# Performance work log

Hardware: AMD Instinct MI355X
Metric: run time of the kernel (lower is better)

Reference implementation:

```python
import jax, jax.numpy as jnp
import numpy as np

N, E, SEQ, IN, HID, OUT = 2048, 65536, 5, 32, 64, 16
EPS = 1e-5


def setup_inputs() -> dict:
    ks = jax.random.split(jax.random.key(0), 16)
    def w(k, shape):
        return jax.random.normal(k, shape, jnp.float32) / np.float32(np.sqrt(shape[0]))
    z = lambda n: jnp.zeros((n,), jnp.float32)
    return dict(
        x=jax.random.normal(ks[0], (SEQ, N, IN), jnp.float32),
        edge_weight=jax.random.uniform(ks[1], (E,), jnp.float32),
        Wcz=w(ks[2], (IN, HID)), bcz=z(HID), Wlz=w(ks[3], (2 * HID, HID)), blz=z(HID),
        Wcr=w(ks[4], (IN, HID)), bcr=z(HID), Wlr=w(ks[5], (2 * HID, HID)), blr=z(HID),
        Wch=w(ks[6], (IN, HID)), bch=z(HID), Wlh=w(ks[7], (2 * HID, HID)), blh=z(HID),
        Wred=w(ks[8], (SEQ * HID, HID)), bred=z(HID),
        Wc1=w(ks[9], (HID, HID)), bc1=z(HID), Wc2=w(ks[10], (HID, HID)), bc2=z(HID),
        g1=jnp.ones((HID,), jnp.float32), be1=z(HID),
        g2=jnp.ones((HID,), jnp.float32), be2=z(HID),
        Wout=w(ks[11], (HID, OUT)), bout=z(OUT),
        Wi1=w(ks[12], (2 * HID, HID)), bi1=z(HID),
        Wi2=w(ks[13], (HID, 1)), bi2=z(1),
        edge_index=jax.random.randint(ks[14], (2, E), 0, N),
    )


def _layer_norm(h, g, b):
    mu = jnp.mean(h, -1, keepdims=True)
    var = jnp.mean((h - mu) ** 2, -1, keepdims=True)
    return (h - mu) * jax.lax.rsqrt(var + EPS) * g + b


def _forward(x, edge_weight, Wcz, bcz, Wlz, blz, Wcr, bcr, Wlr, blr,
             Wch, bch, Wlh, blh, Wred, bred, Wc1, bc1, Wc2, bc2,
             g1, be1, g2, be2, Wout, bout, Wi1, bi1, Wi2, bi2, edge_index):
    src, dst = edge_index[0], edge_index[1]
    # GCN symmetric normalization with self-loops (weight 1.0); shared by all convs.
    deg = jax.ops.segment_sum(edge_weight, dst, num_segments=N) + 1.0
    dinv = jax.lax.rsqrt(deg)
    norm = dinv[src] * edge_weight * dinv[dst]  # [E]
    dself = dinv * dinv                          # [N] self-loop coefficient

    def gcn(h, W, b):
        hw = h @ W
        agg = jax.ops.segment_sum(norm[:, None] * hw[src], dst, num_segments=N)
        return agg + dself[:, None] * hw + b

    # TGCN per timestep. The original passes no hidden state, so H resets to 0
    # each call: H_t = (1 - Z) * tanh(candidate); reset gate R is multiplied by
    # H=0 and has no effect (its params get zero gradient, matching torch).
    hs = []
    for t in range(SEQ):  # SEQ=5, fixed small loop
        Zg = jax.nn.sigmoid(gcn(x[t], Wcz, bcz) @ Wlz[:HID] + blz)
        Ht = jnp.tanh(gcn(x[t], Wch, bch) @ Wlh[:HID] + blh)
        hs.append((1.0 - Zg) * Ht)
    h = jnp.stack(hs, axis=1).reshape(N, SEQ * HID)
    h = h @ Wred + bred
    emb = h  # intermediate embeddings for the interaction predictor
    h = gcn(h, Wc1, bc1)
    h = jax.nn.relu(_layer_norm(h, g1, be1))  # dropout = identity in eval
    h = gcn(h, Wc2, bc2)
    h = jax.nn.relu(_layer_norm(h, g2, be2))
    node_pred = h @ Wout + bout
    # InteractionPredictor: cat([e_i, e_j]) @ Wi1 == e_i @ Wi1[:H] + e_j @ Wi1[H:]
    a = emb @ Wi1[:HID]
    bj = emb @ Wi1[HID:]
    hp = jax.nn.relu(a[:, None, :] + bj[None, :, :] + bi1)  # [N, N, HID]
    scores = (hp @ Wi2)[..., 0] + bi2[0]                     # [N, N]
    return node_pred, scores


def reference(x, edge_index, edge_weight, Wcz, bcz, Wlz, blz, Wcr, bcr, Wlr, blr,
              Wch, bch, Wlh, blh, Wred, bred, Wc1, bc1, Wc2, bc2,
              g1, be1, g2, be2, Wout, bout, Wi1, bi1, Wi2, bi2):
    return _forward(x, edge_weight, Wcz, bcz, Wlz, blz, Wcr, bcr, Wlr, blr,
                    Wch, bch, Wlh, blh, Wred, bred, Wc1, bc1, Wc2, bc2,
                    g1, be1, g2, be2, Wout, bout, Wi1, bi1, Wi2, bi2, edge_index)
```

## Files before the change

kernel.cpp:

```cpp
#include <hip/hip_runtime.h>
#include <math.h>

#define N_NODES 2048
#define N_EDGES 65536
#define SEQL 5
#define IN_F 32
#define HID 64
#define OUT_F 16
#define LN_EPS 1e-5f

__global__ void k_deg(const int* __restrict__ ei, const float* __restrict__ ew,
                      float* __restrict__ deg, int* __restrict__ cnt){
    int e = blockIdx.x * 256 + threadIdx.x;
    if (e < N_EDGES){
        int d = ei[N_EDGES + e];
        atomicAdd(&deg[d], ew[e]);
        atomicAdd(&cnt[d], 1);
    }
}

__global__ void k_scan_wcomb(const float* __restrict__ deg, const int* __restrict__ cnt,
                             float* __restrict__ dinv, float* __restrict__ dself, int* __restrict__ rowptr,
                             const float* __restrict__ Wcz, const float* __restrict__ Wlz,
                             const float* __restrict__ bcz, const float* __restrict__ blz,
                             const float* __restrict__ Wch, const float* __restrict__ Wlh,
                             const float* __restrict__ bch, const float* __restrict__ blh,
                             float* __restrict__ Wzp, float* __restrict__ Whp, float* __restrict__ bUV){
    int b = blockIdx.x, t = threadIdx.x;
    if (b == 0){
        __shared__ int s[1024];
        int n0 = 2*t, n1 = 2*t + 1;
        float d0 = deg[n0] + 1.f, d1 = deg[n1] + 1.f;
        float i0 = 1.f / sqrtf(d0), i1 = 1.f / sqrtf(d1);
        dinv[n0] = i0; dinv[n1] = i1;
        dself[n0] = i0*i0; dself[n1] = i1*i1;
        int a0 = cnt[n0], a1 = cnt[n1];
        s[t] = a0 + a1;
        __syncthreads();
        for (int off = 1; off < 1024; off <<= 1){
            int v = (t >= off) ? s[t - off] : 0;
            __syncthreads();
            s[t] += v;
            __syncthreads();
        }
        int pe = (t == 0) ? 0 : s[t-1];
        rowptr[n0] = pe;
        rowptr[n1] = pe + a0;
        if (t == 1023) rowptr[2048] = s[1023];
    } else {
        const float* Wc = (b == 1) ? Wcz : Wch;
        const float* Wl = (b == 1) ? Wlz : Wlh;
        const float* bc = (b == 1) ? bcz : bch;
        const float* bl = (b == 1) ? blz : blh;
        float* Wp = (b == 1) ? Wzp : Whp;
        for (int idx = t; idx < IN_F*HID; idx += 1024){
            int i = idx >> 6, f = idx & 63;
            float s = 0.f;
            for (int k = 0; k < HID; ++k) s += Wc[i*HID+k] * Wl[k*HID+f];
            Wp[idx] = s;
        }
        if (t < HID){
            float s = bl[t];
            for (int k = 0; k < HID; ++k) s += bc[k] * Wl[k*HID+t];
            bUV[(b-1)*HID + t] = s;
        }
    }
}

__global__ void k_csr(const int* __restrict__ ei, const float* __restrict__ ew,
                      const float* __restrict__ dinv, const int* __restrict__ rowptr,
                      int* __restrict__ fill, int* __restrict__ csrc, float* __restrict__ cnrm){
    int e = blockIdx.x * 256 + threadIdx.x;
    if (e < N_EDGES){
        int s = ei[e], d = ei[N_EDGES + e];
        int pos = rowptr[d] + atomicAdd(&fill[d], 1);
        csrc[pos] = s;
        cnrm[pos] = dinv[s] * ew[e] * dinv[d];
    }
}

__global__ __launch_bounds__(256) void k_aggx(const float* __restrict__ x, const float* __restrict__ dself,
        const int* __restrict__ rowptr, const int* __restrict__ csrc, const float* __restrict__ cnrm,
        float* __restrict__ aggX){
    int n = blockIdx.x;
    int tid = threadIdx.x;
    int slot = tid >> 5, f = tid & 31;
    __shared__ float part[8][SEQL][IN_F];
    float acc[SEQL] = {0.f, 0.f, 0.f, 0.f, 0.f};
    int beg = rowptr[n], end = rowptr[n+1];
    for (int p = beg + slot; p < end; p += 8){
        int s = csrc[p]; float c = cnrm[p];
        #pragma unroll
        for (int t = 0; t < SEQL; ++t)
            acc[t] += c * x[(t*N_NODES + s)*IN_F + f];
    }
    #pragma unroll
    for (int t = 0; t < SEQL; ++t) part[slot][t][f] = acc[t];
    __syncthreads();
    if (tid < SEQL*IN_F){
        int t = tid >> 5, ff = tid & 31;
        float s = dself[n] * x[(t*N_NODES + n)*IN_F + ff];
        #pragma unroll
        for (int sl = 0; sl < 8; ++sl) s += part[sl][t][ff];
        aggX[n*(SEQL*IN_F) + tid] = s;
    }
}

__global__ __launch_bounds__(320) void k_gate2(const float* __restrict__ aggX, const float* __restrict__ bUV,
        const float* __restrict__ Wzp, const float* __restrict__ Whp,
        const float* __restrict__ Wred, const float* __restrict__ bred,
        const float* __restrict__ Wi1, const float* __restrict__ bi1, const float* __restrict__ Wc1,
        float* __restrict__ emb, float* __restrict__ ag, float* __restrict__ bjp,
        float* __restrict__ hw1){
    int n = blockIdx.x;
    int f = threadIdx.x & 63;
    int t = threadIdx.x >> 6;
    __shared__ float axs[SEQL][IN_F];
    __shared__ float hs[SEQL][HID];
    __shared__ float part[SEQL][HID];
    if (threadIdx.x < SEQL*IN_F) ((float*)axs)[threadIdx.x] = aggX[n*(SEQL*IN_F) + threadIdx.x];
    __syncthreads();
    float zz = bUV[f], hh = bUV[HID + f];
    #pragma unroll
    for (int i = 0; i < IN_F; ++i){
        float a = axs[t][i];
        zz += a * Wzp[i*HID + f];
        hh += a * Whp[i*HID + f];
    }
    float z = 1.f / (1.f + expf(-zz));
    hs[t][f] = (1.f - z) * tanhf(hh);
    __syncthreads();
    float pp = 0.f;
    #pragma unroll
    for (int k = 0; k < HID; ++k) pp += hs[t][k] * Wred[(t*HID + k)*HID + f];
    part[t][f] = pp;
    __syncthreads();
    if (t == 0){
        float hred = bred[f] + part[0][f] + part[1][f] + part[2][f] + part[3][f] + part[4][f];
        emb[n*HID + f] = hred;
        hs[0][f] = hred;
    }
    __syncthreads();
    if (t < 3){
        const float* W = (t == 0) ? Wi1 : (t == 1) ? (Wi1 + HID*HID) : Wc1;
        float acc = (t == 1) ? bi1[f] : 0.f;
        #pragma unroll
        for (int k = 0; k < HID; ++k) acc += hs[0][k] * W[k*HID + f];
        float* O = (t == 0) ? ag : (t == 1) ? bjp : hw1;
        O[n*HID + f] = acc;
    }
}

__global__ __launch_bounds__(256) void k_gcn1(
                       const float* __restrict__ hw1, const float* __restrict__ dself,
                       const int* __restrict__ rowptr, const int* __restrict__ csrc, const float* __restrict__ cnrm,
                       const float* __restrict__ bc1, const float* __restrict__ g1, const float* __restrict__ be1,
                       const float* __restrict__ Wc2, float* __restrict__ hw2){
    int n = blockIdx.x;
    int f = threadIdx.x & 63;
    int w = threadIdx.x >> 6;
    int beg = rowptr[n], end = rowptr[n+1];
    __shared__ float red[4][HID];
    __shared__ float hsh[HID];
    float agg = 0.f;
    for (int p = beg + w; p < end; p += 4) agg += cnrm[p] * hw1[csrc[p]*HID + f];
    red[w][f] = agg;
    __syncthreads();
    if (w == 0){
        float g = red[0][f] + red[1][f] + red[2][f] + red[3][f]
                + dself[n] * hw1[n*HID + f] + bc1[f];
        float sum = g;
        for (int o = 32; o > 0; o >>= 1) sum += __shfl_xor(sum, o, 64);
        float mu = sum * (1.f/64.f);
        float d = g - mu;
        float vs = d * d;
        for (int o = 32; o > 0; o >>= 1) vs += __shfl_xor(vs, o, 64);
        float var = vs * (1.f/64.f);
        float h = d * (1.f / sqrtf(var + LN_EPS)) * g1[f] + be1[f];
        hsh[f] = fmaxf(h, 0.f);
    }
    __syncthreads();
    float s = 0.f;
    #pragma unroll
    for (int k = 0; k < 16; ++k) s += hsh[w*16 + k] * Wc2[(w*16 + k)*HID + f];
    red[w][f] = s;
    __syncthreads();
    if (w == 0) hw2[n*HID + f] = red[0][f] + red[1][f] + red[2][f] + red[3][f];
}

__global__ __launch_bounds__(256) void k_gcn2(
                       const float* __restrict__ hw2, const float* __restrict__ dself,
                       const int* __restrict__ rowptr, const int* __restrict__ csrc, const float* __restrict__ cnrm,
                       const float* __restrict__ bc2, const float* __restrict__ g2, const float* __restrict__ be2,
                       const float* __restrict__ Wout, const float* __restrict__ bout, float* __restrict__ outp){
    int n = blockIdx.x;
    int f = threadIdx.x & 63;
    int w = threadIdx.x >> 6;
    int beg = rowptr[n], end = rowptr[n+1];
    __shared__ float red[4][HID];
    __shared__ float hsh[HID];
    float agg = 0.f;
    for (int p = beg + w; p < end; p += 4) agg += cnrm[p] * hw2[csrc[p]*HID + f];
    red[w][f] = agg;
    __syncthreads();
    if (w == 0){
        float g = red[0][f] + red[1][f] + red[2][f] + red[3][f]
                + dself[n] * hw2[n*HID + f] + bc2[f];
        float sum = g;
        for (int o = 32; o > 0; o >>= 1) sum += __shfl_xor(sum, o, 64);
        float mu = sum * (1.f/64.f);
        float d = g - mu;
        float vs = d * d;
        for (int o = 32; o > 0; o >>= 1) vs += __shfl_xor(vs, o, 64);
        float var = vs * (1.f/64.f);
        float h = d * (1.f / sqrtf(var + LN_EPS)) * g2[f] + be2[f];
        hsh[f] = fmaxf(h, 0.f);
    }
    __syncthreads();
    if (w == 0 && f < OUT_F){
        float s = bout[f];
        #pragma unroll
        for (int k = 0; k < HID; ++k) s += hsh[k] * Wout[k*OUT_F + f];
        outp[n*OUT_F + f] = s;
    }
}

__global__ __launch_bounds__(256) void k_scores(const float* __restrict__ ag, const float* __restrict__ bjp,
                         const float* __restrict__ Wi2, const float* __restrict__ bi2,
                         float* __restrict__ outs){
    __shared__ __align__(16) float bs[64][68];
    __shared__ __align__(16) float as[16][68];
    __shared__ __align__(16) float wv[64];
    int tid = threadIdx.x;
    int j0 = blockIdx.x * 64;
    int i0 = blockIdx.y * 16;
    for (int idx = tid; idx < 1024; idx += 256){
        int jj = idx >> 4, c = idx & 15;
        float4 v = *(const float4*)&bjp[(j0 + jj)*HID + c*4];
        *(float4*)&bs[jj][c*4] = v;
    }
    {   int ii = tid >> 4, c = tid & 15;
        float4 v = *(const float4*)&ag[(i0 + ii)*HID + c*4];
        *(float4*)&as[ii][c*4] = v;
    }
    if (tid < 64) wv[tid] = Wi2[tid];
    __syncthreads();
    int tj = tid & 63;
    int w = tid >> 6;
    float bi2v = bi2[0];
    float acc0 = 0.f, acc1 = 0.f, acc2 = 0.f, acc3 = 0.f;
    #pragma unroll
    for (int c = 0; c < 16; ++c){
        float4 bv = *(float4*)&bs[tj][c*4];
        float4 w4 = *(float4*)&wv[c*4];
        float4 a0 = *(float4*)&as[w*4 + 0][c*4];
        float4 a1 = *(float4*)&as[w*4 + 1][c*4];
        float4 a2 = *(float4*)&as[w*4 + 2][c*4];
        float4 a3 = *(float4*)&as[w*4 + 3][c*4];
        acc0 += fmaxf(a0.x+bv.x,0.f)*w4.x + fmaxf(a0.y+bv.y,0.f)*w4.y
              + fmaxf(a0.z+bv.z,0.f)*w4.z + fmaxf(a0.w+bv.w,0.f)*w4.w;
        acc1 += fmaxf(a1.x+bv.x,0.f)*w4.x + fmaxf(a1.y+bv.y,0.f)*w4.y
              + fmaxf(a1.z+bv.z,0.f)*w4.z + fmaxf(a1.w+bv.w,0.f)*w4.w;
        acc2 += fmaxf(a2.x+bv.x,0.f)*w4.x + fmaxf(a2.y+bv.y,0.f)*w4.y
              + fmaxf(a2.z+bv.z,0.f)*w4.z + fmaxf(a2.w+bv.w,0.f)*w4.w;
        acc3 += fmaxf(a3.x+bv.x,0.f)*w4.x + fmaxf(a3.y+bv.y,0.f)*w4.y
              + fmaxf(a3.z+bv.z,0.f)*w4.z + fmaxf(a3.w+bv.w,0.f)*w4.w;
    }
    long ro = (long)(i0 + w*4) * N_NODES + j0 + tj;
    outs[ro                ] = acc0 + bi2v;
    outs[ro +     N_NODES  ] = acc1 + bi2v;
    outs[ro + 2L* N_NODES  ] = acc2 + bi2v;
    outs[ro + 3L* N_NODES  ] = acc3 + bi2v;
}

extern "C" void kernel_launch(void* const* d_in, const int* in_sizes, int n_in,
                              void* d_out, int out_size, void* d_ws, size_t ws_size,
                              hipStream_t stream){
    const float* x   = (const float*)d_in[0];
    const float* ew  = (const float*)d_in[1];
    const float* Wcz = (const float*)d_in[2];  const float* bcz = (const float*)d_in[3];
    const float* Wlz = (const float*)d_in[4];  const float* blz = (const float*)d_in[5];
    const float* Wch = (const float*)d_in[10]; const float* bch = (const float*)d_in[11];
    const float* Wlh = (const float*)d_in[12]; const float* blh = (const float*)d_in[13];
    const float* Wred= (const float*)d_in[14]; const float* bred= (const float*)d_in[15];
    const float* Wc1 = (const float*)d_in[16]; const float* bc1 = (const float*)d_in[17];
    const float* Wc2 = (const float*)d_in[18]; const float* bc2 = (const float*)d_in[19];
    const float* g1  = (const float*)d_in[20]; const float* be1 = (const float*)d_in[21];
    const float* g2  = (const float*)d_in[22]; const float* be2 = (const float*)d_in[23];
    const float* Wout= (const float*)d_in[24]; const float* bout= (const float*)d_in[25];
    const float* Wi1 = (const float*)d_in[26]; const float* bi1 = (const float*)d_in[27];
    const float* Wi2 = (const float*)d_in[28]; const float* bi2 = (const float*)d_in[29];
    const int*  ei  = (const int*)d_in[30];

    char* w = (char*)d_ws;
    float* deg    = (float*)(w + 0);
    int*   cnt    = (int*)  (w + 8192);
    int*   fill   = (int*)  (w + 16384);
    int*   rowptr = (int*)  (w + 24576);
    float* dinv   = (float*)(w + 36864);
    float* dself  = (float*)(w + 45056);
    int*   csrc   = (int*)  (w + 53248);
    float* cnrm   = (float*)(w + 315392);
    float* Wzp    = (float*)(w + 577536);
    float* Whp    = (float*)(w + 585728);
    float* bUV    = (float*)(w + 593920);
    float* aggX   = (float*)(w + 595968);
    float* emb    = (float*)(w + 1906688);
    float* ag     = emb + N_NODES*HID;
    float* bjp    = ag  + N_NODES*HID;
    float* hw1    = bjp + N_NODES*HID;
    float* hw2    = hw1 + N_NODES*HID;

    hipMemsetAsync(d_ws, 0, 24576, stream);
    k_deg<<<N_EDGES/256, 256, 0, stream>>>(ei, ew, deg, cnt);
    k_scan_wcomb<<<3, 1024, 0, stream>>>(deg, cnt, dinv, dself, rowptr,
                                         Wcz, Wlz, bcz, blz, Wch, Wlh, bch, blh,
                                         Wzp, Whp, bUV);
    k_csr<<<N_EDGES/256, 256, 0, stream>>>(ei, ew, dinv, rowptr, fill, csrc, cnrm);
    k_aggx<<<N_NODES, 256, 0, stream>>>(x, dself, rowptr, csrc, cnrm, aggX);
    k_gate2<<<N_NODES, 320, 0, stream>>>(aggX, bUV, Wzp, Whp, Wred, bred, Wi1, bi1, Wc1,
                                         emb, ag, bjp, hw1);
    k_gcn1<<<N_NODES, 256, 0, stream>>>(hw1, dself, rowptr, csrc, cnrm, bc1, g1, be1, Wc2, hw2);
    k_gcn2<<<N_NODES, 256, 0, stream>>>(hw2, dself, rowptr, csrc, cnrm, bc2, g2, be2, Wout, bout,
                                        (float*)d_out);
    dim3 sg(N_NODES/64, N_NODES/16);
    k_scores<<<sg, 256, 0, stream>>>(ag, bjp, Wi2, bi2, (float*)d_out + N_NODES*OUT_F);
}
```

Before: 218.8 us.

## Fuse all stages into one persistent cooperative kernel with grid syncs

Replaces the memset and eight separate kernel launches with a single cooperative kernel of 256 blocks of 512 threads. Stages are separated by grid.sync(), and each block loops over 8 nodes or tiles per stage. The aggX and emb intermediates are no longer written to global memory; the gate computation reads aggregated features from shared memory. This removes launch gaps and the memset, but adds grid-wide barriers and gives low occupancy (256 blocks) for the gather and score phases, which could cost throughput.

```diff
diff --git a/kernel.cpp b/kernel.cpp
--- a/kernel.cpp
+++ b/kernel.cpp
@@ -1,5 +1,8 @@
 #include <hip/hip_runtime.h>
+#include <hip/hip_cooperative_groups.h>
 #include <math.h>
+
+namespace cg = cooperative_groups;
 
 #define N_NODES 2048
 #define N_EDGES 65536
@@ -8,321 +11,332 @@
 #define HID 64
 #define OUT_F 16
 #define LN_EPS 1e-5f
-
-__global__ void k_deg(const int* __restrict__ ei, const float* __restrict__ ew,
-                      float* __restrict__ deg, int* __restrict__ cnt){
-    int e = blockIdx.x * 256 + threadIdx.x;
-    if (e < N_EDGES){
-        int d = ei[N_EDGES + e];
-        atomicAdd(&deg[d], ew[e]);
-        atomicAdd(&cnt[d], 1);
-    }
-}
-
-__global__ void k_scan_wcomb(const float* __restrict__ deg, const int* __restrict__ cnt,
-                             float* __restrict__ dinv, float* __restrict__ dself, int* __restrict__ rowptr,
-                             const float* __restrict__ Wcz, const float* __restrict__ Wlz,
-                             const float* __restrict__ bcz, const float* __restrict__ blz,
-                             const float* __restrict__ Wch, const float* __restrict__ Wlh,
-                             const float* __restrict__ bch, const float* __restrict__ blh,
-                             float* __restrict__ Wzp, float* __restrict__ Whp, float* __restrict__ bUV){
-    int b = blockIdx.x, t = threadIdx.x;
-    if (b == 0){
-        __shared__ int s[1024];
-        int n0 = 2*t, n1 = 2*t + 1;
-        float d0 = deg[n0] + 1.f, d1 = deg[n1] + 1.f;
-        float i0 = 1.f / sqrtf(d0), i1 = 1.f / sqrtf(d1);
-        dinv[n0] = i0; dinv[n1] = i1;
-        dself[n0] = i0*i0; dself[n1] = i1*i1;
-        int a0 = cnt[n0], a1 = cnt[n1];
-        s[t] = a0 + a1;
+#define NBLK 256
+#define NTHR 512
+
+struct Params {
+    const float *x, *ew;
+    const float *Wcz, *bcz, *Wlz, *blz;
+    const float *Wch, *bch, *Wlh, *blh;
+    const float *Wred, *bred, *Wc1, *bc1, *Wc2, *bc2;
+    const float *g1, *be1, *g2, *be2, *Wout, *bout;
+    const float *Wi1, *bi1, *Wi2, *bi2;
+    const int *ei;
+    float *deg; int *cnt; int *fill; int *rowptr;
+    float *dinv, *dself; int *csrc; float *cnrm;
+    float *Wzp, *Whp, *bUV;
+    float *ag, *bjp, *hw1, *hw2;
+    float *outp, *outs;
+};
+
+__global__ __launch_bounds__(NTHR) void k_mega(Params P){
+    cg::grid_group grid = cg::this_grid();
+    const int tid = threadIdx.x, blk = blockIdx.x;
+    const int gid = blk * NTHR + tid;
+    __shared__ float LP[6656];
+
+    if (gid < N_NODES){ P.deg[gid] = 0.f; P.cnt[gid] = 0; P.fill[gid] = 0; }
+    grid.sync();
+
+    if (gid < N_EDGES){
+        int d = P.ei[N_EDGES + gid];
+        atomicAdd(&P.deg[d], P.ew[gid]);
+        atomicAdd(&P.cnt[d], 1);
+    }
+    grid.sync();
+
+    if (blk == 0){
+        int* sc = (int*)LP;
+        int base = tid * 4;
+        int c0 = P.cnt[base], c1 = P.cnt[base+1], c2 = P.cnt[base+2], c3 = P.cnt[base+3];
+        int ts = c0 + c1 + c2 + c3;
+        sc[tid] = ts;
         __syncthreads();
-        for (int off = 1; off < 1024; off <<= 1){
-            int v = (t >= off) ? s[t - off] : 0;
-            __syncthreads();
-            s[t] += v;
-            __syncthreads();
-        }
-        int pe = (t == 0) ? 0 : s[t-1];
-        rowptr[n0] = pe;
-        rowptr[n1] = pe + a0;
-        if (t == 1023) rowptr[2048] = s[1023];
-    } else {
-        const float* Wc = (b == 1) ? Wcz : Wch;
-        const float* Wl = (b == 1) ? Wlz : Wlh;
-        const float* bc = (b == 1) ? bcz : bch;
-        const float* bl = (b == 1) ? blz : blh;
-        float* Wp = (b == 1) ? Wzp : Whp;
-        for (int idx = t; idx < IN_F*HID; idx += 1024){
+        for (int off = 1; off < NTHR; off <<= 1){
+            int v = (tid >= off) ? sc[tid - off] : 0;
+            __syncthreads();
+            sc[tid] += v;
+            __syncthreads();
+        }
+        int exc = sc[tid] - ts;
+        P.rowptr[base]   = exc;
+        P.rowptr[base+1] = exc + c0;
+        P.rowptr[base+2] = exc + c0 + c1;
+        P.rowptr[base+3] = exc + c0 + c1 + c2;
+        if (tid == NTHR-1) P.rowptr[N_NODES] = sc[tid];
+    } else if (blk == 1 || blk == 2){
+        const float* Wc = (blk == 1) ? P.Wcz : P.Wch;
+        const float* Wl = (blk == 1) ? P.Wlz : P.Wlh;
+        const float* bc = (blk == 1) ? P.bcz : P.bch;
+        const float* bl = (blk == 1) ? P.blz : P.blh;
+        float* Wp = (blk == 1) ? P.Wzp : P.Whp;
+        for (int idx = tid; idx < IN_F*HID; idx += NTHR){
             int i = idx >> 6, f = idx & 63;
             float s = 0.f;
             for (int k = 0; k < HID; ++k) s += Wc[i*HID+k] * Wl[k*HID+f];
             Wp[idx] = s;
         }
-        if (t < HID){
-            float s = bl[t];
-            for (int k = 0; k < HID; ++k) s += bc[k] * Wl[k*HID+t];
-            bUV[(b-1)*HID + t] = s;
-        }
-    }
-}
-
-__global__ void k_csr(const int* __restrict__ ei, const float* __restrict__ ew,
-                      const float* __restrict__ dinv, const int* __restrict__ rowptr,
-                      int* __restrict__ fill, int* __restrict__ csrc, float* __restrict__ cnrm){
-    int e = blockIdx.x * 256 + threadIdx.x;
-    if (e < N_EDGES){
-        int s = ei[e], d = ei[N_EDGES + e];
-        int pos = rowptr[d] + atomicAdd(&fill[d], 1);
-        csrc[pos] = s;
-        cnrm[pos] = dinv[s] * ew[e] * dinv[d];
-    }
-}
-
-__global__ __launch_bounds__(256) void k_aggx(const float* __restrict__ x, const float* __restrict__ dself,
-        const int* __restrict__ rowptr, const int* __restrict__ csrc, const float* __restrict__ cnrm,
-        float* __restrict__ aggX){
-    int n = blockIdx.x;
-    int tid = threadIdx.x;
-    int slot = tid >> 5, f = tid & 31;
-    __shared__ float part[8][SEQL][IN_F];
-    float acc[SEQL] = {0.f, 0.f, 0.f, 0.f, 0.f};
-    int beg = rowptr[n], end = rowptr[n+1];
-    for (int p = beg + slot; p < end; p += 8){
-        int s = csrc[p]; float c = cnrm[p];
+        if (tid < HID){
+            float s = bl[tid];
+            for (int k = 0; k < HID; ++k) s += bc[k] * Wl[k*HID+tid];
+            P.bUV[(blk-1)*HID + tid] = s;
+        }
+    } else if (blk == 3){
+        int base = tid * 4;
         #pragma unroll
-        for (int t = 0; t < SEQL; ++t)
-            acc[t] += c * x[(t*N_NODES + s)*IN_F + f];
-    }
-    #pragma unroll
-    for (int t = 0; t < SEQL; ++t) part[slot][t][f] = acc[t];
-    __syncthreads();
-    if (tid < SEQL*IN_F){
-        int t = tid >> 5, ff = tid & 31;
-        float s = dself[n] * x[(t*N_NODES + n)*IN_F + ff];
-        #pragma unroll
-        for (int sl = 0; sl < 8; ++sl) s += part[sl][t][ff];
-        aggX[n*(SEQL*IN_F) + tid] = s;
-    }
-}
-
-__global__ __launch_bounds__(320) void k_gate2(const float* __restrict__ aggX, const float* __restrict__ bUV,
-        const float* __restrict__ Wzp, const float* __restrict__ Whp,
-        const float* __restrict__ Wred, const float* __restrict__ bred,
-        const float* __restrict__ Wi1, const float* __restrict__ bi1, const float* __restrict__ Wc1,
-        float* __restrict__ emb, float* __restrict__ ag, float* __restrict__ bjp,
-        float* __restrict__ hw1){
-    int n = blockIdx.x;
-    int f = threadIdx.x & 63;
-    int t = threadIdx.x >> 6;
-    __shared__ float axs[SEQL][IN_F];
-    __shared__ float hs[SEQL][HID];
-    __shared__ float part[SEQL][HID];
-    if (threadIdx.x < SEQL*IN_F) ((float*)axs)[threadIdx.x] = aggX[n*(SEQL*IN_F) + threadIdx.x];
-    __syncthreads();
-    float zz = bUV[f], hh = bUV[HID + f];
-    #pragma unroll
-    for (int i = 0; i < IN_F; ++i){
-        float a = axs[t][i];
-        zz += a * Wzp[i*HID + f];
-        hh += a * Whp[i*HID + f];
-    }
-    float z = 1.f / (1.f + expf(-zz));
-    hs[t][f] = (1.f - z) * tanhf(hh);
-    __syncthreads();
-    float pp = 0.f;
-    #pragma unroll
-    for (int k = 0; k < HID; ++k) pp += hs[t][k] * Wred[(t*HID + k)*HID + f];
-    part[t][f] = pp;
-    __syncthreads();
-    if (t == 0){
-        float hred = bred[f] + part[0][f] + part[1][f] + part[2][f] + part[3][f] + part[4][f];
-        emb[n*HID + f] = hred;
-        hs[0][f] = hred;
-    }
-    __syncthreads();
-    if (t < 3){
-        const float* W = (t == 0) ? Wi1 : (t == 1) ? (Wi1 + HID*HID) : Wc1;
-        float acc = (t == 1) ? bi1[f] : 0.f;
-        #pragma unroll
-        for (int k = 0; k < HID; ++k) acc += hs[0][k] * W[k*HID + f];
-        float* O = (t == 0) ? ag : (t == 1) ? bjp : hw1;
-        O[n*HID + f] = acc;
-    }
-}
-
-__global__ __launch_bounds__(256) void k_gcn1(
-                       const float* __restrict__ hw1, const float* __restrict__ dself,
-                       const int* __restrict__ rowptr, const int* __restrict__ csrc, const float* __restrict__ cnrm,
-                       const float* __restrict__ bc1, const float* __restrict__ g1, const float* __restrict__ be1,
-                       const float* __restrict__ Wc2, float* __restrict__ hw2){
-    int n = blockIdx.x;
-    int f = threadIdx.x & 63;
-    int w = threadIdx.x >> 6;
-    int beg = rowptr[n], end = rowptr[n+1];
-    __shared__ float red[4][HID];
-    __shared__ float hsh[HID];
-    float agg = 0.f;
-    for (int p = beg + w; p < end; p += 4) agg += cnrm[p] * hw1[csrc[p]*HID + f];
-    red[w][f] = agg;
-    __syncthreads();
-    if (w == 0){
-        float g = red[0][f] + red[1][f] + red[2][f] + red[3][f]
-                + dself[n] * hw1[n*HID + f] + bc1[f];
-        float sum = g;
-        for (int o = 32; o > 0; o >>= 1) sum += __shfl_xor(sum, o, 64);
-        float mu = sum * (1.f/64.f);
-        float d = g - mu;
-        float vs = d * d;
-        for (int o = 32; o > 0; o >>= 1) vs += __shfl_xor(vs, o, 64);
-        float var = vs * (1.f/64.f);
-        float h = d * (1.f / sqrtf(var + LN_EPS)) * g1[f] + be1[f];
-        hsh[f] = fmaxf(h, 0.f);
-    }
-    __syncthreads();
-    float s = 0.f;
-    #pragma unroll
-    for (int k = 0; k < 16; ++k) s += hsh[w*16 + k] * Wc2[(w*16 + k)*HID + f];
-    red[w][f] = s;
-    __syncthreads();
-    if (w == 0) hw2[n*HID + f] = red[0][f] + red[1][f] + red[2][f] + red[3][f];
-}
-
-__global__ __launch_bounds__(256) void k_gcn2(
-                       const float* __restrict__ hw2, const float* __restrict__ dself,
-                       const int* __restrict__ rowptr, const int* __restrict__ csrc, const float* __restrict__ cnrm,
-                       const float* __restrict__ bc2, const float* __restrict__ g2, const float* __restrict__ be2,
-                       const float* __restrict__ Wout, const float* __restrict__ bout, float* __restrict__ outp){
-    int n = blockIdx.x;
-    int f = threadIdx.x & 63;
-    int w = threadIdx.x >> 6;
-    int beg = rowptr[n], end = rowptr[n+1];
-    __shared__ float red[4][HID];
-    __shared__ float hsh[HID];
-    float agg = 0.f;
-    for (int p = beg + w; p < end; p += 4) agg += cnrm[p] * hw2[csrc[p]*HID + f];
-    red[w][f] = agg;
-    __syncthreads();
-    if (w == 0){
-        float g = red[0][f] + red[1][f] + red[2][f] + red[3][f]
-                + dself[n] * hw2[n*HID + f] + bc2[f];
-        float sum = g;
-        for (int o = 32; o > 0; o >>= 1) sum += __shfl_xor(sum, o, 64);
-        float mu = sum * (1.f/64.f);
-        float d = g - mu;
-        float vs = d * d;
-        for (int o = 32; o > 0; o >>= 1) vs += __shfl_xor(vs, o, 64);
-        float var = vs * (1.f/64.f);
-        float h = d * (1.f / sqrtf(var + LN_EPS)) * g2[f] + be2[f];
-        hsh[f] = fmaxf(h, 0.f);
-    }
-    __syncthreads();
-    if (w == 0 && f < OUT_F){
-        float s = bout[f];
-        #pragma unroll
-        for (int k = 0; k < HID; ++k) s += hsh[k] * Wout[k*OUT_F + f];
-        outp[n*OUT_F + f] = s;
-    }
-}
-
-__global__ __launch_bounds__(256) void k_scores(const float* __restrict__ ag, const float* __restrict__ bjp,
-                         const float* __restrict__ Wi2, const float* __restrict__ bi2,
-                         float* __restrict__ outs){
-    __shared__ __align__(16) float bs[64][68];
-    __shared__ __align__(16) float as[16][68];
-    __shared__ __align__(16) float wv[64];
-    int tid = threadIdx.x;
-    int j0 = blockIdx.x * 64;
-    int i0 = blockIdx.y * 16;
-    for (int idx = tid; idx < 1024; idx += 256){
-        int jj = idx >> 4, c = idx & 15;
-        float4 v = *(const float4*)&bjp[(j0 + jj)*HID + c*4];
-        *(float4*)&bs[jj][c*4] = v;
-    }
-    {   int ii = tid >> 4, c = tid & 15;
-        float4 v = *(const float4*)&ag[(i0 + ii)*HID + c*4];
-        *(float4*)&as[ii][c*4] = v;
-    }
-    if (tid < 64) wv[tid] = Wi2[tid];
-    __syncthreads();
-    int tj = tid & 63;
-    int w = tid >> 6;
-    float bi2v = bi2[0];
-    float acc0 = 0.f, acc1 = 0.f, acc2 = 0.f, acc3 = 0.f;
-    #pragma unroll
-    for (int c = 0; c < 16; ++c){
-        float4 bv = *(float4*)&bs[tj][c*4];
-        float4 w4 = *(float4*)&wv[c*4];
-        float4 a0 = *(float4*)&as[w*4 + 0][c*4];
-        float4 a1 = *(float4*)&as[w*4 + 1][c*4];
-        float4 a2 = *(float4*)&as[w*4 + 2][c*4];
-        float4 a3 = *(float4*)&as[w*4 + 3][c*4];
-        acc0 += fmaxf(a0.x+bv.x,0.f)*w4.x + fmaxf(a0.y+bv.y,0.f)*w4.y
-              + fmaxf(a0.z+bv.z,0.f)*w4.z + fmaxf(a0.w+bv.w,0.f)*w4.w;
-        acc1 += fmaxf(a1.x+bv.x,0.f)*w4.x + fmaxf(a1.y+bv.y,0.f)*w4.y
-              + fmaxf(a1.z+bv.z,0.f)*w4.z + fmaxf(a1.w+bv.w,0.f)*w4.w;
-        acc2 += fmaxf(a2.x+bv.x,0.f)*w4.x + fmaxf(a2.y+bv.y,0.f)*w4.y
-              + fmaxf(a2.z+bv.z,0.f)*w4.z + fmaxf(a2.w+bv.w,0.f)*w4.w;
-        acc3 += fmaxf(a3.x+bv.x,0.f)*w4.x + fmaxf(a3.y+bv.y,0.f)*w4.y
-              + fmaxf(a3.z+bv.z,0.f)*w4.z + fmaxf(a3.w+bv.w,0.f)*w4.w;
-    }
-    long ro = (long)(i0 + w*4) * N_NODES + j0 + tj;
-    outs[ro                ] = acc0 + bi2v;
-    outs[ro +     N_NODES  ] = acc1 + bi2v;
-    outs[ro + 2L* N_NODES  ] = acc2 + bi2v;
-    outs[ro + 3L* N_NODES  ] = acc3 + bi2v;
+        for (int k = 0; k < 4; ++k){
+            int i = base + k;
+            float di = 1.f / sqrtf(P.deg[i] + 1.f);
+            P.dinv[i] = di; P.dself[i] = di * di;
+        }
+    }
+    grid.sync();
+
+    if (gid < N_EDGES){
+        int s = P.ei[gid], d = P.ei[N_EDGES + gid];
+        int pos = P.rowptr[d] + atomicAdd(&P.fill[d], 1);
+        P.csrc[pos] = s;
+        P.cnrm[pos] = P.dinv[s] * P.ew[gid] * P.dinv[d];
+    }
+    grid.sync();
+
+    {
+        float* part = LP;
+        float* axs  = LP + 2560;
+        float* hs   = LP + 2720;
+        float* pw   = LP + 3040;
+        float* hemb = LP + 3360;
+        const int slot = tid >> 5, f5 = tid & 31;
+        const int f = tid & 63, t = tid >> 6;
+        for (int rep = 0; rep < 8; ++rep){
+            int n = (rep << 8) + blk;
+            __syncthreads();
+            int beg = P.rowptr[n], end = P.rowptr[n+1];
+            float a0=0.f, a1=0.f, a2=0.f, a3=0.f, a4=0.f;
+            for (int p = beg + slot; p < end; p += 16){
+                int s = P.csrc[p]; float c = P.cnrm[p];
+                a0 += c * P.x[(0*N_NODES + s)*IN_F + f5];
+                a1 += c * P.x[(1*N_NODES + s)*IN_F + f5];
+                a2 += c * P.x[(2*N_NODES + s)*IN_F + f5];
+                a3 += c * P.x[(3*N_NODES + s)*IN_F + f5];
+                a4 += c * P.x[(4*N_NODES + s)*IN_F + f5];
+            }
+            part[(slot*SEQL + 0)*IN_F + f5] = a0;
+            part[(slot*SEQL + 1)*IN_F + f5] = a1;
+            part[(slot*SEQL + 2)*IN_F + f5] = a2;
+            part[(slot*SEQL + 3)*IN_F + f5] = a3;
+            part[(slot*SEQL + 4)*IN_F + f5] = a4;
+            __syncthreads();
+            if (tid < SEQL*IN_F){
+                int tt = tid >> 5, ff = tid & 31;
+                float s = P.dself[n] * P.x[(tt*N_NODES + n)*IN_F + ff];
+                #pragma unroll
+                for (int sl = 0; sl < 16; ++sl) s += part[(sl*SEQL + tt)*IN_F + ff];
+                axs[tt*IN_F + ff] = s;
+            }
+            __syncthreads();
+            if (t < SEQL){
+                float zz = P.bUV[f], hh = P.bUV[HID + f];
+                #pragma unroll
+                for (int i = 0; i < IN_F; ++i){
+                    float a = axs[t*IN_F + i];
+                    zz += a * P.Wzp[i*HID + f];
+                    hh += a * P.Whp[i*HID + f];
+                }
+                float z = 1.f / (1.f + expf(-zz));
+                hs[t*HID + f] = (1.f - z) * tanhf(hh);
+            }
+            __syncthreads();
+            if (t < SEQL){
+                float pp = 0.f;
+                #pragma unroll
+                for (int k = 0; k < HID; ++k) pp += hs[t*HID + k] * P.Wred[(t*HID + k)*HID + f];
+                pw[t*HID + f] = pp;
+            }
+            __syncthreads();
+            if (tid < HID){
+                float hr = P.bred[tid];
+                #pragma unroll
+                for (int t2 = 0; t2 < SEQL; ++t2) hr += pw[t2*HID + tid];
+                hemb[tid] = hr;
+            }
+            __syncthreads();
+            if (t < 3){
+                const float* W = (t == 0) ? P.Wi1 : (t == 1) ? (P.Wi1 + HID*HID) : P.Wc1;
+                float acc = (t == 1) ? P.bi1[f] : 0.f;
+                #pragma unroll
+                for (int k = 0; k < HID; ++k) acc += hemb[k] * W[k*HID + f];
+                float* O = (t == 0) ? P.ag : (t == 1) ? P.bjp : P.hw1;
+                O[n*HID + f] = acc;
+            }
+        }
+    }
+    grid.sync();
+
+    {
+        float* red8 = LP;
+        float* hsh  = LP + 512;
+        const int f = tid & 63, w = tid >> 6;
+        for (int rep = 0; rep < 8; ++rep){
+            int n = (rep << 8) + blk;
+            __syncthreads();
+            int beg = P.rowptr[n], end = P.rowptr[n+1];
+            float agg = 0.f;
+            for (int p = beg + w; p < end; p += 8) agg += P.cnrm[p] * P.hw1[P.csrc[p]*HID + f];
+            red8[w*HID + f] = agg;
+            __syncthreads();
+            if (w == 0){
+                float g = P.bc1[f] + P.dself[n] * P.hw1[n*HID + f];
+                #pragma unroll
+                for (int k = 0; k < 8; ++k) g += red8[k*HID + f];
+                float sum = g;
+                for (int o = 32; o > 0; o >>= 1) sum += __shfl_xor(sum, o, 64);
+                float mu = sum * (1.f/64.f);
+                float d = g - mu;
+                float vs = d * d;
+                for (int o = 32; o > 0; o >>= 1) vs += __shfl_xor(vs, o, 64);
+                float var = vs * (1.f/64.f);
+                float h = d * (1.f / sqrtf(var + LN_EPS)) * P.g1[f] + P.be1[f];
+                hsh[f] = fmaxf(h, 0.f);
+            }
+            __syncthreads();
+            float s = 0.f;
+            #pragma unroll
+            for (int k = 0; k < 8; ++k) s += hsh[w*8 + k] * P.Wc2[(w*8 + k)*HID + f];
+            red8[w*HID + f] = s;
+            __syncthreads();
+            if (w == 0){
+                float o = 0.f;
+                #pragma unroll
+                for (int k = 0; k < 8; ++k) o += red8[k*HID + f];
+                P.hw2[n*HID + f] = o;
+            }
+        }
+    }
+    grid.sync();
+
+    {
+        float* red8 = LP;
+        float* hsh  = LP + 512;
+        const int f = tid & 63, w = tid >> 6;
+        for (int rep = 0; rep < 8; ++rep){
+            int n = (rep << 8) + blk;
+            __syncthreads();
+            int beg = P.rowptr[n], end = P.rowptr[n+1];
+            float agg = 0.f;
+            for (int p = beg + w; p < end; p += 8) agg += P.cnrm[p] * P.hw2[P.csrc[p]*HID + f];
+            red8[w*HID + f] = agg;
+            __syncthreads();
+            if (w == 0){
+                float g = P.bc2[f] + P.dself[n] * P.hw2[n*HID + f];
+                #pragma unroll
+                for (int k = 0; k < 8; ++k) g += red8[k*HID + f];
+                float sum = g;
+                for (int o = 32; o > 0; o >>= 1) sum += __shfl_xor(sum, o, 64);
+                float mu = sum * (1.f/64.f);
+                float d = g - mu;
+                float vs = d * d;
+                for (int o = 32; o > 0; o >>= 1) vs += __shfl_xor(vs, o, 64);
+                float var = vs * (1.f/64.f);
+                float h = d * (1.f / sqrtf(var + LN_EPS)) * P.g2[f] + P.be2[f];
+                hsh[f] = fmaxf(h, 0.f);
+            }
+            __syncthreads();
+            if (w == 0 && f < OUT_F){
+                float s = P.bout[f];
+                #pragma unroll
+                for (int k = 0; k < HID; ++k) s += hsh[k] * P.Wout[k*OUT_F + f];
+                P.outp[n*OUT_F + f] = s;
+            }
+        }
+    }
+    {
+        float* bs = LP;
+        float* as = LP + 4352;
+        float* wv = LP + 6528;
+        const int tj = tid & 63, w = tid >> 6;
+        float b2v = P.bi2[0];
+        for (int rep = 0; rep < 8; ++rep){
+            int tl = (rep << 8) + blk;
+            int i0 = (tl >> 5) * 32, j0 = (tl & 31) * 64;
+            __syncthreads();
+            for (int idx = tid; idx < 1024; idx += NTHR){
+                int jj = idx >> 4, c = idx & 15;
+                *(float4*)&bs[jj*68 + c*4] = *(const float4*)&P.bjp[(j0 + jj)*HID + c*4];
+            }
+            {
+                int ii = tid >> 4, c = tid & 15;
+                *(float4*)&as[ii*68 + c*4] = *(const float4*)&P.ag[(i0 + ii)*HID + c*4];
+            }
+            if (tid < 64) wv[tid] = P.Wi2[tid];
+            __syncthreads();
+            float acc0 = 0.f, acc1 = 0.f, acc2 = 0.f, acc3 = 0.f;
+            #pragma unroll
+            for (int c = 0; c < 16; ++c){
+                float4 bv = *(float4*)&bs[tj*68 + c*4];
+                float4 w4 = *(float4*)&wv[c*4];
+                float4 r0 = *(float4*)&as[(w*4 + 0)*68 + c*4];
+                float4 r1 = *(float4*)&as[(w*4 + 1)*68 + c*4];
+                float4 r2 = *(float4*)&as[(w*4 + 2)*68 + c*4];
+                float4 r3 = *(float4*)&as[(w*4 + 3)*68 + c*4];
+                acc0 += fmaxf(r0.x+bv.x,0.f)*w4.x + fmaxf(r0.y+bv.y,0.f)*w4.y
+                      + fmaxf(r0.z+bv.z,0.f)*w4.z + fmaxf(r0.w+bv.w,0.f)*w4.w;
+                acc1 += fmaxf(r1.x+bv.x,0.f)*w4.x + fmaxf(r1.y+bv.y,0.f)*w4.y
+                      + fmaxf(r1.z+bv.z,0.f)*w4.z + fmaxf(r1.w+bv.w,0.f)*w4.w;
+                acc2 += fmaxf(r2.x+bv.x,0.f)*w4.x + fmaxf(r2.y+bv.y,0.f)*w4.y
+                      + fmaxf(r2.z+bv.z,0.f)*w4.z + fmaxf(r2.w+bv.w,0.f)*w4.w;
+                acc3 += fmaxf(r3.x+bv.x,0.f)*w4.x + fmaxf(r3.y+bv.y,0.f)*w4.y
+                      + fmaxf(r3.z+bv.z,0.f)*w4.z + fmaxf(r3.w+bv.w,0.f)*w4.w;
+            }
+            long ro = (long)(i0 + w*4) * N_NODES + j0 + tj;
+            P.outs[ro               ] = acc0 + b2v;
+            P.outs[ro +     N_NODES ] = acc1 + b2v;
+            P.outs[ro + 2L* N_NODES ] = acc2 + b2v;
+            P.outs[ro + 3L* N_NODES ] = acc3 + b2v;
+        }
+    }
 }
 
 extern "C" void kernel_launch(void* const* d_in, const int* in_sizes, int n_in,
                               void* d_out, int out_size, void* d_ws, size_t ws_size,
                               hipStream_t stream){
-    const float* x   = (const float*)d_in[0];
-    const float* ew  = (const float*)d_in[1];
-    const float* Wcz = (const float*)d_in[2];  const float* bcz = (const float*)d_in[3];
-    const float* Wlz = (const float*)d_in[4];  const float* blz = (const float*)d_in[5];
-    const float* Wch = (const float*)d_in[10]; const float* bch = (const float*)d_in[11];
-    const float* Wlh = (const float*)d_in[12]; const float* blh = (const float*)d_in[13];
-    const float* Wred= (const float*)d_in[14]; const float* bred= (const float*)d_in[15];
-    const float* Wc1 = (const float*)d_in[16]; const float* bc1 = (const float*)d_in[17];
-    const float* Wc2 = (const float*)d_in[18]; const float* bc2 = (const float*)d_in[19];
-    const float* g1  = (const float*)d_in[20]; const float* be1 = (const float*)d_in[21];
-    const float* g2  = (const float*)d_in[22]; const float* be2 = (const float*)d_in[23];
-    const float* Wout= (const float*)d_in[24]; const float* bout= (const float*)d_in[25];
-    const float* Wi1 = (const float*)d_in[26]; const float* bi1 = (const float*)d_in[27];
-    const float* Wi2 = (const float*)d_in[28]; const float* bi2 = (const float*)d_in[29];
-    const int*  ei  = (const int*)d_in[30];
-
-    char* w = (char*)d_ws;
-    float* deg    = (float*)(w + 0);
-    int*   cnt    = (int*)  (w + 8192);
-    int*   fill   = (int*)  (w + 16384);
-    int*   rowptr = (int*)  (w + 24576);
-    float* dinv   = (float*)(w + 36864);
-    float* dself  = (float*)(w + 45056);
-    int*   csrc   = (int*)  (w + 53248);
-    float* cnrm   = (float*)(w + 315392);
-    float* Wzp    = (float*)(w + 577536);
-    float* Whp    = (float*)(w + 585728);
-    float* bUV    = (float*)(w + 593920);
-    float* aggX   = (float*)(w + 595968);
-    float* emb    = (float*)(w + 1906688);
-    float* ag     = emb + N_NODES*HID;
-    float* bjp    = ag  + N_NODES*HID;
-    float* hw1    = bjp + N_NODES*HID;
-    float* hw2    = hw1 + N_NODES*HID;
-
-    hipMemsetAsync(d_ws, 0, 24576, stream);
-    k_deg<<<N_EDGES/256, 256, 0, stream>>>(ei, ew, deg, cnt);
-    k_scan_wcomb<<<3, 1024, 0, stream>>>(deg, cnt, dinv, dself, rowptr,
-                                         Wcz, Wlz, bcz, blz, Wch, Wlh, bch, blh,
-                                         Wzp, Whp, bUV);
-    k_csr<<<N_EDGES/256, 256, 0, stream>>>(ei, ew, dinv, rowptr, fill, csrc, cnrm);
-    k_aggx<<<N_NODES, 256, 0, stream>>>(x, dself, rowptr, csrc, cnrm, aggX);
-    k_gate2<<<N_NODES, 320, 0, stream>>>(aggX, bUV, Wzp, Whp, Wred, bred, Wi1, bi1, Wc1,
-                                         emb, ag, bjp, hw1);
-    k_gcn1<<<N_NODES, 256, 0, stream>>>(hw1, dself, rowptr, csrc, cnrm, bc1, g1, be1, Wc2, hw2);
-    k_gcn2<<<N_NODES, 256, 0, stream>>>(hw2, dself, rowptr, csrc, cnrm, bc2, g2, be2, Wout, bout,
-                                        (float*)d_out);
-    dim3 sg(N_NODES/64, N_NODES/16);
-    k_scores<<<sg, 256, 0, stream>>>(ag, bjp, Wi2, bi2, (float*)d_out + N_NODES*OUT_F);
+    Params P;
+    P.x   = (const float*)d_in[0];
+    P.ew  = (const float*)d_in[1];
+    P.Wcz = (const float*)d_in[2];  P.bcz = (const float*)d_in[3];
+    P.Wlz = (const float*)d_in[4];  P.blz = (const float*)d_in[5];
+    P.Wch = (const float*)d_in[10]; P.bch = (const float*)d_in[11];
+    P.Wlh = (const float*)d_in[12]; P.blh = (const float*)d_in[13];
+    P.Wred= (const float*)d_in[14]; P.bred= (const float*)d_in[15];
+    P.Wc1 = (const float*)d_in[16]; P.bc1 = (const float*)d_in[17];
+    P.Wc2 = (const float*)d_in[18]; P.bc2 = (const float*)d_in[19];
+    P.g1  = (const float*)d_in[20]; P.be1 = (const float*)d_in[21];
+    P.g2  = (const float*)d_in[22]; P.be2 = (const float*)d_in[23];
+    P.Wout= (const float*)d_in[24]; P.bout= (const float*)d_in[25];
+    P.Wi1 = (const float*)d_in[26]; P.bi1 = (const float*)d_in[27];
+    P.Wi2 = (const float*)d_in[28]; P.bi2 = (const float*)d_in[29];
+    P.ei  = (const int*)d_in[30];
+
+    float* w = (float*)d_ws;
+    P.deg    = w;
+    P.cnt    = (int*)(w + 2048);
+    P.fill   = (int*)(w + 4096);
+    P.rowptr = (int*)(w + 6144);
+    P.dinv   = w + 8704;
+    P.dself  = w + 10752;
+    P.csrc   = (int*)(w + 12800);
+    P.cnrm   = w + 78336;
+    P.Wzp    = w + 143872;
+    P.Whp    = w + 145920;
+    P.bUV    = w + 147968;
+    P.ag     = w + 148096;
+    P.bjp    = w + 279168;
+    P.hw1    = w + 410240;
+    P.hw2    = w + 541312;
+    P.outp   = (float*)d_out;
+    P.outs   = (float*)d_out + N_NODES*OUT_F;
+
+    void* args[] = { &P };
+    hipLaunchCooperativeKernel((const void*)k_mega, dim3(NBLK), dim3(NTHR),
+                               args, 0, stream);
 }
```

Measured after the change: 812.9 us. 3.71x slower.
